# Kernel optimization log

Hardware: AMD Instinct MI355X
Metric: run time of the kernel (lower is better)

## Reference

```python
import jax, jax.numpy as jnp
import numpy as np
from jax import lax

DIM, HEADS, POOL = 512, 8, 16
HD = DIM // HEADS
SCALE = HD ** -0.5


def _cbs(x, w, s, b, d=1, g=1):
    """Conv2d(bias=False, pad=d*(k-1)//2) + folded BN (scale,bias) + SiLU."""
    k = w.shape[-1]
    p = d * (k - 1) // 2
    y = lax.conv_general_dilated(x, w, (1, 1), [(p, p), (p, p)],
                                 rhs_dilation=(d, d), feature_group_count=g,
                                 dimension_numbers=("NCHW", "OIHW", "NCHW"))
    y = y * s[None, :, None, None] + b[None, :, None, None]
    return y * jax.nn.sigmoid(y)  # SiLU


def _forward(x, w01, s01, b01, w02, s02, b02, w03, s03, b03,
             w12, s12, b12, w13, s13, b13, w22, s22, b22, w23, s23, b23,
             w3, s3, b3, wkv, skv, bkv, wfc1, bfc1, wfc2, bfc2):
    bsz, c, h, w = x.shape
    # ---- _MutilScal ----
    a01 = _cbs(x, w01, s01, b01)                       # [b,128,h,w]
    a03 = _cbs(_cbs(a01, w02, s02, b02, d=3, g=128), w03, s03, b03)
    a13 = _cbs(_cbs(a01, w12, s12, b12, d=5, g=128), w13, s13, b13)
    a23 = _cbs(_cbs(a01, w22, s22, b22, d=7, g=128), w23, s23, b23)
    attn = _cbs(a03 + a13 + a23, w3, s3, b3) * x       # [b,512,h,w]
    # AdaptiveAvgPool2d(POOL): exact block mean since h,w divisible by POOL
    pooled = attn.reshape(bsz, c, POOL, h // POOL, POOL, w // POOL).mean(axis=(3, 5))
    kv = _cbs(pooled, wkv, skv, bkv)                   # [b,1024,16,16]
    # ---- pooled cross-attention ----
    n, n1 = h * w, POOL * POOL
    q = x.reshape(bsz, HEADS, HD, n).transpose(0, 1, 3, 2)          # [b,H,n,d]
    kvr = kv.reshape(bsz, 2, HEADS, HD, n1)
    k = kvr[:, 0].transpose(0, 1, 3, 2)                              # [b,H,n1,d]
    v = kvr[:, 1].transpose(0, 1, 3, 2)                              # [b,H,n1,d]
    dots = jnp.einsum("bhnd,bhmd->bhnm", q, k) * SCALE
    a = jax.nn.softmax(dots, axis=-1)
    o = jnp.einsum("bhnm,bhmd->bhnd", a, v)                          # [b,H,n,d]
    attn_out = o.transpose(0, 1, 3, 2).reshape(bsz, c, h, w)
    # ---- SE channel gate ----
    gap = x.mean(axis=(2, 3))                                        # [b,c]
    y = jnp.clip(gap @ wfc1[:, :, 0, 0].T + bfc1, 0.0, 6.0)          # ReLU6
    gate = jax.nn.sigmoid(y @ wfc2[:, :, 0, 0].T + bfc2)             # [b,c]
    c_attn = gate[:, :, None, None] * x
    return attn_out + c_attn


def setup_inputs() -> dict:
    key = jax.random.key(0)
    ks = jax.random.split(key, 32)
    ki = iter(ks)
    f = jnp.float32

    def rn(shape, scale=0.05):
        return (jax.random.normal(next(ki), shape, dtype=f) * scale)

    inp = {"x": jax.random.normal(next(ki), (8, DIM, 64, 64), dtype=f)}
    inp.update(w01=rn((128, 512, 1, 1)), s01=jnp.ones((128,), f), b01=rn((128,)))
    inp.update(w02=rn((128, 1, 3, 3)), s02=jnp.ones((128,), f), b02=rn((128,)))
    inp.update(w03=rn((512, 128, 1, 1)), s03=jnp.ones((512,), f), b03=rn((512,)))
    inp.update(w12=rn((128, 1, 3, 3)), s12=jnp.ones((128,), f), b12=rn((128,)))
    inp.update(w13=rn((512, 128, 1, 1)), s13=jnp.ones((512,), f), b13=rn((512,)))
    inp.update(w22=rn((128, 1, 3, 3)), s22=jnp.ones((128,), f), b22=rn((128,)))
    inp.update(w23=rn((512, 128, 1, 1)), s23=jnp.ones((512,), f), b23=rn((512,)))
    inp.update(w3=rn((512, 512, 1, 1)), s3=jnp.ones((512,), f), b3=rn((512,)))
    inp.update(wkv=rn((1024, 512, 1, 1)), skv=jnp.ones((1024,), f), bkv=rn((1024,)))
    inp.update(wfc1=rn((128, 512, 1, 1)), bfc1=rn((128,)))
    inp.update(wfc2=rn((512, 128, 1, 1)), bfc2=rn((512,)))
    return inp


def reference(x, w01, s01, b01, w02, s02, b02, w03, s03, b03,
              w12, s12, b12, w13, s13, b13, w22, s22, b22, w23, s23, b23,
              w3, s3, b3, wkv, skv, bkv, wfc1, bfc1, wfc2, bfc2):
    return _forward(x, w01, s01, b01, w02, s02, b02, w03, s03, b03,
                    w12, s12, b12, w13, s13, b13, w22, s22, b22, w23, s23, b23,
                    w3, s3, b3, wkv, skv, bkv, wfc1, bfc1, wfc2, bfc2)
```

## Files before the change

kernel.cpp:

```cpp
#include <hip/hip_runtime.h>
#include <cstddef>


static __device__ __forceinline__ float silu_f(float v) {
  return v / (1.f + __expf(-v));
}

typedef __attribute__((ext_vector_type(8))) short short8v;
typedef __attribute__((ext_vector_type(4))) float f32x4;

union FragU { unsigned u[4]; short8v v; uint4 q; };

static __device__ __forceinline__ unsigned short f2bf(float f) {
  unsigned u = __builtin_bit_cast(unsigned, f);
  u += 0x7fffu + ((u >> 16) & 1u);
  return (unsigned short)(u >> 16);
}
static __device__ __forceinline__ unsigned packbf(float lo, float hi) {
  return (unsigned)f2bf(lo) | ((unsigned)f2bf(hi) << 16);
}
static __device__ __forceinline__ float bf_lo(unsigned w) {
  return __builtin_bit_cast(float, w << 16);
}
static __device__ __forceinline__ float bf_hi(unsigned w) {
  return __builtin_bit_cast(float, w & 0xffff0000u);
}

static __device__ __forceinline__ void gload16(const unsigned* gsrc, unsigned* ldst) {
  __builtin_amdgcn_global_load_lds(
      (const __attribute__((address_space(1))) unsigned*)gsrc,
      (__attribute__((address_space(3))) unsigned*)ldst, 16, 0, 0);
}

static __device__ __forceinline__ void stage_tile_g(const unsigned* __restrict__ src,
                                                    unsigned* dst, int tid) {
  gload16(src + 4 * tid, dst + 4 * tid);
  gload16(src + 4 * (tid + 512), dst + 4 * (tid + 512));
}

static __device__ __forceinline__ short8v load_frag4(const unsigned* P, int ksg, int pos) {
  FragU f;
  f.q = *(const uint4*)(P + (((ksg << 7) + pos) << 2));
  return f.v;
}

static __device__ __forceinline__ void xload16(const float* __restrict__ src, int ld,
                                               int tid, float v[16]) {
  const int pos = tid & 127, kg = tid >> 7;
  const float* p = src + pos + (size_t)(kg * 16) * ld;
#pragma unroll
  for (int i = 0; i < 16; ++i) v[i] = p[(size_t)i * ld];
}
static __device__ __forceinline__ void xload16_sum2(const float* __restrict__ a,
                                                    const float* __restrict__ b2, int ld,
                                                    int tid, float v[16]) {
  const int pos = tid & 127, kg = tid >> 7;
  const float* pA = a + pos + (size_t)(kg * 16) * ld;
  const float* pB = b2 + pos + (size_t)(kg * 16) * ld;
#pragma unroll
  for (int i = 0; i < 16; ++i) v[i] = pA[(size_t)i * ld] + pB[(size_t)i * ld];
}
static __device__ __forceinline__ void xwrite16(const float v[16], unsigned* Xp, int tid) {
  const int pos = tid & 127, kg = tid >> 7;
#pragma unroll
  for (int i2 = 0; i2 < 4; ++i2) {
    const int kq = kg * 4 + i2;
    const int r4 = (kq & 3) + ((kq >> 3) << 2);
    const int sub = (kq >> 2) & 1;
    uint2 wv;
    wv.x = packbf(v[i2 * 4 + 0], v[i2 * 4 + 1]);
    wv.y = packbf(v[i2 * 4 + 2], v[i2 * 4 + 3]);
    *(uint2*)(Xp + (((r4 << 7) + pos) << 2) + sub * 2) = wv;
  }
}

static __device__ __forceinline__ void stage_x_pack(const float* __restrict__ src, int ld,
                                                    unsigned* Xp, int tid) {
  float v[16];
  xload16(src, ld, tid, v);
  xwrite16(v, Xp, tid);
}

#define GEMM_IDS                                            \
  const int tid = threadIdx.x;                              \
  const int w = tid >> 6, lane = tid & 63;                  \
  const int g = lane >> 4, nl = lane & 15;                  \
  const int wr = w >> 1, wc = w & 1;

#define GEMM_KSTEP_B(ACC, XB, WB)                                                  \
  _Pragma("unroll")                                                                \
  for (int ks = 0; ks < 2; ++ks) {                                                 \
    const short8v a0 = load_frag4(WB, ks * 4 + g, wr * 32 + nl);                   \
    const short8v a1 = load_frag4(WB, ks * 4 + g, wr * 32 + 16 + nl);              \
    _Pragma("unroll")                                                              \
    for (int jj = 0; jj < 4; ++jj) {                                               \
      const short8v bfr = load_frag4(XB, ks * 4 + g, wc * 64 + jj * 16 + nl);      \
      ACC[0][jj] = __builtin_amdgcn_mfma_f32_16x16x32_bf16(a0, bfr, ACC[0][jj], 0, 0, 0); \
      ACC[1][jj] = __builtin_amdgcn_mfma_f32_16x16x32_bf16(a1, bfr, ACC[1][jj], 0, 0, 0); \
    }                                                                              \
  }

__global__ __launch_bounds__(256)
void prepack_w_kernel(const float* __restrict__ w01, const float* __restrict__ w03,
                      const float* __restrict__ w13, const float* __restrict__ w23,
                      const float* __restrict__ w3, const float* __restrict__ wkv,
                      unsigned* __restrict__ img)
{
  const int t = blockIdx.x;
  const float* W; int K; int tile; unsigned* base;
  if (t < 8)       { W = w01; K = 512; tile = t;      base = img; }
  else if (t < 16) { W = w03; K = 128; tile = t - 8;  base = img + 32768; }
  else if (t < 24) { W = w13; K = 128; tile = t - 16; base = img + 65536; }
  else if (t < 32) { W = w23; K = 128; tile = t - 24; base = img + 98304; }
  else if (t < 64) { W = w3;  K = 512; tile = t - 32; base = img + 131072; }
  else             { W = wkv; K = 512; tile = t - 64; base = img + 262144; }
  const int nk = K >> 6;
  const int to = tile / nk, tk = tile - to * nk;
  unsigned* dst = base + (size_t)tile * 4096;
  for (int wi = threadIdx.x; wi < 4096; wi += 256) {
    const int r4 = wi >> 9, pos = (wi >> 2) & 127, sub = (wi >> 1) & 1, j = wi & 1;
    const int kq = (r4 & 3) + sub * 4 + ((r4 >> 2) << 3);
    const int k = tk * 64 + 4 * kq + 2 * j;
    const int oc = to * 128 + pos;
    dst[wi] = packbf(W[(size_t)oc * K + k], W[(size_t)oc * K + k + 1]);
  }
}

__global__ __launch_bounds__(512)
void gemm_a01_kernel(const float* __restrict__ X, const unsigned* __restrict__ Wimg,
                     const float* __restrict__ sc, const float* __restrict__ bi,
                     unsigned* __restrict__ A01p)
{
  const int b = blockIdx.z, p0 = blockIdx.x * 128;
  GEMM_IDS
  __shared__ unsigned Xp[2][4096], Wp[2][4096];
  const float* Xbase = X + (size_t)b * 512 * 4096 + p0;

  f32x4 acc[2][4];
#pragma unroll
  for (int i = 0; i < 2; ++i)
#pragma unroll
    for (int jj = 0; jj < 4; ++jj) acc[i][jj] = (f32x4){0.f, 0.f, 0.f, 0.f};

  {
    float vx[16];
    xload16(Xbase, 4096, tid, vx);
    stage_tile_g(Wimg, Wp[0], tid);
    xwrite16(vx, Xp[0], tid);
  }
  __syncthreads();

  for (int st = 0; st < 8; ++st) {
    const int cur = st & 1;
    float vn[16];
    if (st < 7) {
      xload16(Xbase + (size_t)((st + 1) * 64) * 4096, 4096, tid, vn);
      stage_tile_g(Wimg + (size_t)(st + 1) * 4096, Wp[cur ^ 1], tid);
    }
    GEMM_KSTEP_B(acc, Xp[cur], Wp[cur])
    if (st < 7) xwrite16(vn, Xp[cur ^ 1], tid);
    __syncthreads();
  }

#pragma unroll
  for (int i = 0; i < 2; ++i) {
    const int base = wr * 32 + i * 16 + 4 * g;
    const float s0_ = sc[base + 0], b0_ = bi[base + 0];
    const float s1_ = sc[base + 1], b1_ = bi[base + 1];
    const float s2_ = sc[base + 2], b2_ = bi[base + 2];
    const float s3_ = sc[base + 3], b3_ = bi[base + 3];
#pragma unroll
    for (int jj = 0; jj < 4; ++jj) {
      const int pos = p0 + wc * 64 + jj * 16 + nl;
      const float v0 = silu_f(s0_ * acc[i][jj][0] + b0_);
      const float v1 = silu_f(s1_ * acc[i][jj][1] + b1_);
      const float v2 = silu_f(s2_ * acc[i][jj][2] + b2_);
      const float v3 = silu_f(s3_ * acc[i][jj][3] + b3_);
      A01p[((size_t)b * 64 + (base >> 1)) * 4096 + pos]     = packbf(v0, v1);
      A01p[((size_t)b * 64 + (base >> 1) + 1) * 4096 + pos] = packbf(v2, v3);
    }
  }
}

__global__ __launch_bounds__(256)
void dwconv_pack_kernel(const unsigned* __restrict__ A01p, unsigned* __restrict__ Timg,
                        const float* __restrict__ w02, const float* __restrict__ s02, const float* __restrict__ b02,
                        const float* __restrict__ w12, const float* __restrict__ s12, const float* __restrict__ b12,
                        const float* __restrict__ w22, const float* __restrict__ s22, const float* __restrict__ b22)
{
  const int br = blockIdx.z;
  const int yb = blockIdx.y;
  const int b = yb >> 4, t16 = yb & 15, kstep = t16 >> 3, mm = t16 & 7;
  const int kq = (mm & 3) + ((mm >> 2) << 3);
  const int cbase = kstep * 64 + kq * 4;
  const int p = blockIdx.x * 256 + threadIdx.x;
  const int y = p >> 6, xx = p & 63;
  const int d = 3 + 2 * br;

  const float* wsel = br == 0 ? w02 : (br == 1 ? w12 : w22);
  const float* ssel = br == 0 ? s02 : (br == 1 ? s12 : s22);
  const float* bsel = br == 0 ? b02 : (br == 1 ? b12 : b22);

  float sum[8] = {};
  const unsigned* plane0 = A01p + ((size_t)b * 64 + (cbase >> 1)) * 4096;

#pragma unroll
  for (int u = -1; u <= 1; ++u) {
    const int yv = y + u * d;
    if ((unsigned)yv < 64u) {
#pragma unroll
      for (int v = -1; v <= 1; ++v) {
        const int xv = xx + v * d;
        if ((unsigned)xv < 64u) {
          const int idx = yv * 64 + xv;
          const int tap = (u + 1) * 3 + (v + 1);
#pragma unroll
          for (int q = 0; q < 4; ++q) {
            const int sub = q >> 1, jw = q & 1;
            const unsigned wv = plane0[(size_t)(sub * 8 + jw) * 4096 + idx];
            const int ch = cbase + sub * 16 + jw * 2;
            sum[q * 2 + 0] += wsel[(ch + 0) * 9 + tap] * bf_lo(wv);
            sum[q * 2 + 1] += wsel[(ch + 1) * 9 + tap] * bf_hi(wv);
          }
        }
      }
    }
  }

  unsigned wout[4];
#pragma unroll
  for (int h = 0; h < 4; ++h) {
    const int ch = cbase + (h >> 1) * 16 + (h & 1) * 2;
    const float va = silu_f(ssel[ch] * sum[h * 2] + bsel[ch]);
    const float vb = silu_f(ssel[ch + 1] * sum[h * 2 + 1] + bsel[ch + 1]);
    wout[h] = packbf(va, vb);
  }
  const int tile = ((br * 8 + b) * 2 + kstep) * 32 + (p >> 7);
  *(uint4*)(Timg + (size_t)tile * 4096 + (((mm << 7) + (p & 127)) << 2)) = *(uint4*)wout;
}

__global__ __launch_bounds__(512)
void gemm3branch_img_kernel(const unsigned* __restrict__ Timg, const unsigned* __restrict__ Wimg3,
                            const float* __restrict__ s0, const float* __restrict__ s1, const float* __restrict__ s2,
                            const float* __restrict__ b0, const float* __restrict__ b1, const float* __restrict__ b2,
                            unsigned* __restrict__ Bimg)
{
  const int b = blockIdx.z, pt = blockIdx.x, oc0 = blockIdx.y * 128;
  GEMM_IDS
  __shared__ unsigned Xp[2][4096], Wp[2][4096];

  float sum[2][4][4] = {};
  f32x4 acc[2][4];
#pragma unroll
  for (int i = 0; i < 2; ++i)
#pragma unroll
    for (int jj = 0; jj < 4; ++jj) acc[i][jj] = (f32x4){0.f, 0.f, 0.f, 0.f};

#define SRC_X3(st) (Timg + (((size_t)(((st) >> 1) * 8 + b) * 2 + ((st) & 1)) * 32 + pt) * 4096)
#define SRC_W3(st) (Wimg3 + (size_t)((st) >> 1) * 32768 + ((size_t)(oc0 >> 7) * 2 + ((st) & 1)) * 4096)

  stage_tile_g(SRC_X3(0), Xp[0], tid);
  stage_tile_g(SRC_W3(0), Wp[0], tid);
  __syncthreads();

  for (int st = 0; st < 6; ++st) {
    const int cur = st & 1;
    if (st < 5) {
      stage_tile_g(SRC_X3(st + 1), Xp[cur ^ 1], tid);
      stage_tile_g(SRC_W3(st + 1), Wp[cur ^ 1], tid);
    }
    GEMM_KSTEP_B(acc, Xp[cur], Wp[cur])
    if (st & 1) {
      const int brn = st >> 1;
      const float* ss = brn == 0 ? s0 : (brn == 1 ? s1 : s2);
      const float* bs = brn == 0 ? b0 : (brn == 1 ? b1 : b2);
#pragma unroll
      for (int i = 0; i < 2; ++i) {
        const int base = oc0 + wr * 32 + i * 16 + 4 * g;
#pragma unroll
        for (int r = 0; r < 4; ++r) {
          const float s = ss[base + r], bb = bs[base + r];
#pragma unroll
          for (int jj = 0; jj < 4; ++jj) {
            sum[i][jj][r] += silu_f(s * acc[i][jj][r] + bb);
            acc[i][jj][r] = 0.f;
          }
        }
      }
    }
    __syncthreads();
  }
#undef SRC_X3
#undef SRC_W3

#pragma unroll
  for (int i = 0; i < 2; ++i) {
    const int ol = wr * 32 + i * 16 + 4 * g;
    const int kstep_g = (oc0 + ol) >> 6;
    const int kin = ol & 63;
    const int kq2 = kin >> 2;
    const int r4 = (kq2 & 3) + ((kq2 >> 3) << 2);
    const int sub = (kq2 >> 2) & 1;
#pragma unroll
    for (int jj = 0; jj < 4; ++jj) {
      const int pos = wc * 64 + jj * 16 + nl;
      uint2 wv;
      wv.x = packbf(sum[i][jj][0], sum[i][jj][1]);
      wv.y = packbf(sum[i][jj][2], sum[i][jj][3]);
      *(uint2*)(Bimg + ((size_t)(b * 8 + kstep_g) * 32 + pt) * 4096 + (((r4 << 7) + pos) << 2) + sub * 2) = wv;
    }
  }
}

__global__ __launch_bounds__(512)
void gemm_pool_img_kernel(const unsigned* __restrict__ Bimg, const unsigned* __restrict__ W3img,
                          const float* __restrict__ sc, const float* __restrict__ bi,
                          const float* __restrict__ xin, float* __restrict__ pooled2)
{
  const int b = blockIdx.z, pt = blockIdx.x, oc0 = blockIdx.y * 128;
  const int p0 = pt * 128;
  const float* xb = xin + (size_t)b * 512 * 4096;
  GEMM_IDS
  __shared__ unsigned Xp[2][4096], Wp[2][4096];

  f32x4 acc[2][4];
#pragma unroll
  for (int i = 0; i < 2; ++i)
#pragma unroll
    for (int jj = 0; jj < 4; ++jj) acc[i][jj] = (f32x4){0.f, 0.f, 0.f, 0.f};

#define SRC_XP(st) (Bimg + ((size_t)(b * 8 + (st)) * 32 + pt) * 4096)
#define SRC_WP(st) (W3img + ((size_t)(oc0 >> 7) * 8 + (st)) * 4096)

  stage_tile_g(SRC_XP(0), Xp[0], tid);
  stage_tile_g(SRC_WP(0), Wp[0], tid);
  __syncthreads();

  for (int st = 0; st < 8; ++st) {
    const int cur = st & 1;
    if (st < 7) {
      stage_tile_g(SRC_XP(st + 1), Xp[cur ^ 1], tid);
      stage_tile_g(SRC_WP(st + 1), Wp[cur ^ 1], tid);
    }
    GEMM_KSTEP_B(acc, Xp[cur], Wp[cur])
    __syncthreads();
  }
#undef SRC_XP
#undef SRC_WP

  float* red = (float*)Wp[0];
  for (int e = tid; e < 2048; e += 512) red[e] = 0.f;
  __syncthreads();

#pragma unroll
  for (int i = 0; i < 2; ++i)
#pragma unroll
    for (int r = 0; r < 4; ++r) {
      const int ol = wr * 32 + i * 16 + 4 * g + r;
      const int oc = oc0 + ol;
      const float s = sc[oc], bb = bi[oc];
#pragma unroll
      for (int jj = 0; jj < 4; ++jj) {
        const int p = p0 + wc * 64 + jj * 16 + nl;
        float val = silu_f(s * acc[i][jj][r] + bb) * xb[(size_t)oc * 4096 + p];
        val += __shfl_xor(val, 1, 64);
        val += __shfl_xor(val, 2, 64);
        if ((nl & 3) == 0) {
          const int col = p & 63;
          atomicAdd(&red[ol * 16 + (col >> 2)], val);
        }
      }
    }
  __syncthreads();

  {
    const int ph = pt >> 1;
    float* pdst = pooled2 + (size_t)(pt & 1) * (8ull * 512 * 256);
    for (int e = tid; e < 2048; e += 512) {
      const int ol = e >> 4, pw = e & 15;
      pdst[((size_t)b * 512 + oc0 + ol) * 256 + ph * 16 + pw] = red[e] * (1.f / 16.f);
    }
  }
}

__global__ __launch_bounds__(512)
void gemm_kv_kernel(const float* __restrict__ pooled2, const unsigned* __restrict__ WKVimg,
                    const float* __restrict__ sc, const float* __restrict__ bi,
                    unsigned* __restrict__ Kimg, unsigned* __restrict__ Vimg)
{
  const int b = blockIdx.z, p0 = blockIdx.x * 128, oc0 = blockIdx.y * 128;
  const float* XbA = pooled2 + (size_t)b * 512 * 256 + p0;
  const float* XbB = XbA + 8ull * 512 * 256;
  GEMM_IDS
  __shared__ unsigned Xp[2][4096], Wp[2][4096];

  f32x4 acc[2][4];
#pragma unroll
  for (int i = 0; i < 2; ++i)
#pragma unroll
    for (int jj = 0; jj < 4; ++jj) acc[i][jj] = (f32x4){0.f, 0.f, 0.f, 0.f};

  {
    float vx[16];
    xload16_sum2(XbA, XbB, 256, tid, vx);
    stage_tile_g(WKVimg + (size_t)(oc0 >> 7) * 8 * 4096, Wp[0], tid);
    xwrite16(vx, Xp[0], tid);
  }
  __syncthreads();

  for (int st = 0; st < 8; ++st) {
    const int cur = st & 1;
    float vn[16];
    if (st < 7) {
      xload16_sum2(XbA + (size_t)((st + 1) * 64) * 256, XbB + (size_t)((st + 1) * 64) * 256,
                   256, tid, vn);
      stage_tile_g(WKVimg + ((size_t)(oc0 >> 7) * 8 + st + 1) * 4096, Wp[cur ^ 1], tid);
    }
    GEMM_KSTEP_B(acc, Xp[cur], Wp[cur])
    if (st < 7) xwrite16(vn, Xp[cur ^ 1], tid);
    __syncthreads();
  }

  const bool isK = (oc0 < 512);
#pragma unroll
  for (int i = 0; i < 2; ++i) {
    const int ocb = oc0 + wr * 32 + i * 16 + 4 * g;
#pragma unroll
    for (int jj = 0; jj < 4; ++jj) {
      const int pos = p0 + wc * 64 + jj * 16 + nl;
      float v[4];
#pragma unroll
      for (int r = 0; r < 4; ++r)
        v[r] = silu_f(sc[ocb + r] * acc[i][jj][r] + bi[ocb + r]);
      const int ch = pos >> 7, ml = pos & 127;
      if (isK) {
        const int h = ocb >> 6, d0 = ocb & 63;
        const int kq = d0 >> 2, sub = (kq >> 2) & 1;
        const int r4 = (kq & 3) + ((kq >> 3) << 2);
        unsigned* t = Kimg + ((size_t)(b * 8 + h) * 2 + ch) * 4096;
        uint2 wv;
        wv.x = packbf(v[0] * 0.125f, v[1] * 0.125f);
        wv.y = packbf(v[2] * 0.125f, v[3] * 0.125f);
        *(uint2*)(t + (((r4 << 7) + ml) << 2) + sub * 2) = wv;
      } else {
        const int h = (ocb - 512) >> 6, d0 = (ocb - 512) & 63;
        unsigned* t = Vimg + ((size_t)(b * 8 + h) * 2 + ch) * 4096;
        float ov[4];
#pragma unroll
        for (int r = 0; r < 4; ++r) ov[r] = __shfl_xor(v[r], 1, 64);
        if ((nl & 1) == 0) {
          const int s = (ml >> 1) & 1, m4 = ml >> 2;
#pragma unroll
          for (int r = 0; r < 4; ++r)
            t[((m4 * 64 + d0 + r) << 1) + s] = packbf(v[r], ov[r]);
        }
      }
    }
  }
}

__global__ __launch_bounds__(256)
void gap_kernel(const float* __restrict__ x, float* __restrict__ gap)
{
  const int bc = blockIdx.x;
  const int tid = threadIdx.x;
  const float* p = x + (size_t)bc * 4096;
  float v = 0.f;
#pragma unroll
  for (int j = 0; j < 16; ++j) v += p[j * 256 + tid];
#pragma unroll
  for (int off = 32; off >= 1; off >>= 1) v += __shfl_down(v, off, 64);
  __shared__ float red[4];
  if ((tid & 63) == 0) red[tid >> 6] = v;
  __syncthreads();
  if (tid == 0) gap[bc] = (red[0] + red[1] + red[2] + red[3]) * (1.f / 4096.f);
}

__global__ __launch_bounds__(512)
void se_kernel(const float* __restrict__ gap,
               const float* __restrict__ wfc1, const float* __restrict__ bfc1,
               const float* __restrict__ wfc2, const float* __restrict__ bfc2,
               float* __restrict__ gate)
{
  const int b = blockIdx.x, tid = threadIdx.x;
  __shared__ float ylds[128];
  if (tid < 128) {
    float a = 0.f;
    for (int c = 0; c < 512; ++c) a += gap[b * 512 + c] * wfc1[tid * 512 + c];
    a += bfc1[tid];
    ylds[tid] = fminf(fmaxf(a, 0.f), 6.f);
  }
  __syncthreads();
  float g = 0.f;
  for (int j = 0; j < 128; ++j) g += ylds[j] * wfc2[tid * 128 + j];
  g += bfc2[tid];
  gate[b * 512 + tid] = 1.f / (1.f + __expf(-g));
}

__global__ __launch_bounds__(512)
void attn_mfma_kernel(const float* __restrict__ x, const unsigned* __restrict__ Kimg,
                      const unsigned* __restrict__ Vimg,
                      const float* __restrict__ gate, float* __restrict__ out)
{
  const int b = blockIdx.z, h = blockIdx.y;
  const int n0 = blockIdx.x * 128;
  const int tid = threadIdx.x;
  const int w = tid >> 6, lane = tid & 63;
  const int g = lane >> 4, nl = lane & 15;

  __shared__ unsigned lds[20480];
  unsigned* Qp = lds;
  unsigned* Kb0 = lds + 4096;
  unsigned* Kb1 = lds + 8192;
  unsigned* Vb0 = lds + 12288;
  unsigned* Vb1 = lds + 16384;
  float* Osm = (float*)(lds + 4096);

  const size_t tbase = (size_t)(b * 8 + h) * 2 * 4096;

  stage_tile_g(Kimg + tbase, Kb0, tid);
  stage_tile_g(Vimg + tbase, Vb0, tid);
  stage_x_pack(x + ((size_t)b * 512 + h * 64) * 4096 + n0, 4096, Qp, tid);
  __syncthreads();
  stage_tile_g(Kimg + tbase + 4096, Kb1, tid);
  stage_tile_g(Vimg + tbase + 4096, Vb1, tid);

  float m_run = -1e30f, l_run = 0.f;
  f32x4 o[4];
#pragma unroll
  for (int i = 0; i < 4; ++i) o[i] = (f32x4){0.f, 0.f, 0.f, 0.f};

#pragma unroll
  for (int ch = 0; ch < 2; ++ch) {
    const unsigned* Kp = ch ? Kb1 : Kb0;
    const unsigned* Vp = ch ? Vb1 : Vb0;

    f32x4 s[8];
#pragma unroll
    for (int mb = 0; mb < 8; ++mb) s[mb] = (f32x4){0.f, 0.f, 0.f, 0.f};
#pragma unroll
    for (int ks = 0; ks < 2; ++ks) {
      const short8v qf = load_frag4(Qp, ks * 4 + g, w * 16 + nl);
#pragma unroll
      for (int mb = 0; mb < 8; ++mb) {
        const short8v kf = load_frag4(Kp, ks * 4 + g, mb * 16 + nl);
        s[mb] = __builtin_amdgcn_mfma_f32_16x16x32_bf16(kf, qf, s[mb], 0, 0, 0);
      }
    }

    float cm = -1e30f;
#pragma unroll
    for (int mb = 0; mb < 8; ++mb)
#pragma unroll
      for (int r = 0; r < 4; ++r) cm = fmaxf(cm, s[mb][r]);
    cm = fmaxf(cm, __shfl_xor(cm, 16, 64));
    cm = fmaxf(cm, __shfl_xor(cm, 32, 64));
    const float mnew = fmaxf(m_run, cm);
    const float corr = __expf(m_run - mnew);
    m_run = mnew;
    float cs = 0.f;
#pragma unroll
    for (int mb = 0; mb < 8; ++mb)
#pragma unroll
      for (int r = 0; r < 4; ++r) {
        const float p = __expf(s[mb][r] - mnew);
        s[mb][r] = p;
        cs += p;
      }
    cs += __shfl_xor(cs, 16, 64);
    cs += __shfl_xor(cs, 32, 64);
    l_run = l_run * corr + cs;
#pragma unroll
    for (int db = 0; db < 4; ++db)
#pragma unroll
      for (int r = 0; r < 4; ++r) o[db][r] *= corr;

#pragma unroll
    for (int ks = 0; ks < 4; ++ks) {
      FragU pf;
      pf.u[0] = packbf(s[2 * ks][0],     s[2 * ks][1]);
      pf.u[1] = packbf(s[2 * ks][2],     s[2 * ks][3]);
      pf.u[2] = packbf(s[2 * ks + 1][0], s[2 * ks + 1][1]);
      pf.u[3] = packbf(s[2 * ks + 1][2], s[2 * ks + 1][3]);
#pragma unroll
      for (int db = 0; db < 4; ++db) {
        FragU vf;
        const uint2 lo = *(const uint2*)(Vp + ((8 * ks + g) * 64 + db * 16 + nl) * 2);
        const uint2 hi = *(const uint2*)(Vp + ((8 * ks + 4 + g) * 64 + db * 16 + nl) * 2);
        vf.u[0] = lo.x; vf.u[1] = lo.y; vf.u[2] = hi.x; vf.u[3] = hi.y;
        o[db] = __builtin_amdgcn_mfma_f32_16x16x32_bf16(vf.v, pf.v, o[db], 0, 0, 0);
      }
    }
    __syncthreads();
  }

  const float inv = 1.f / l_run;
#pragma unroll
  for (int db = 0; db < 4; ++db)
#pragma unroll
    for (int r = 0; r < 4; ++r)
      Osm[(db * 16 + 4 * g + r) * 132 + w * 16 + nl] = o[db][r] * inv;
  __syncthreads();

  {
    const int n = tid & 127, t7 = tid >> 7;
    const int jw = t7 >> 1, half = t7 & 1;
#pragma unroll
    for (int i = 0; i < 16; ++i) {
      const int d = t7 + 4 * i;
      const int r4 = (i & 3) + ((i >> 3) << 2);
      const int sub = (i >> 2) & 1;
      const unsigned xw = Qp[(((r4 << 7) + n) << 2) + sub * 2 + jw];
      const float xv = half ? bf_hi(xw) : bf_lo(xw);
      const int c2 = h * 64 + d;
      const size_t off = ((size_t)b * 512 + c2) * 4096 + n0 + n;
      out[off] = Osm[d * 132 + n] + gate[b * 512 + c2] * xv;
    }
  }
}

extern "C" void kernel_launch(void* const* d_in, const int* in_sizes, int n_in,
                              void* d_out, int out_size, void* d_ws, size_t ws_size,
                              hipStream_t stream)
{
  const float* x    = (const float*)d_in[0];
  const float* w01  = (const float*)d_in[1];
  const float* s01  = (const float*)d_in[2];
  const float* b01  = (const float*)d_in[3];
  const float* w02  = (const float*)d_in[4];
  const float* s02  = (const float*)d_in[5];
  const float* b02  = (const float*)d_in[6];
  const float* w03  = (const float*)d_in[7];
  const float* s03  = (const float*)d_in[8];
  const float* b03  = (const float*)d_in[9];
  const float* w12  = (const float*)d_in[10];
  const float* s12  = (const float*)d_in[11];
  const float* b12  = (const float*)d_in[12];
  const float* w13  = (const float*)d_in[13];
  const float* s13  = (const float*)d_in[14];
  const float* b13  = (const float*)d_in[15];
  const float* w22  = (const float*)d_in[16];
  const float* s22  = (const float*)d_in[17];
  const float* b22  = (const float*)d_in[18];
  const float* w23  = (const float*)d_in[19];
  const float* s23  = (const float*)d_in[20];
  const float* b23  = (const float*)d_in[21];
  const float* w3   = (const float*)d_in[22];
  const float* s3   = (const float*)d_in[23];
  const float* b3   = (const float*)d_in[24];
  const float* wkv  = (const float*)d_in[25];
  const float* skv  = (const float*)d_in[26];
  const float* bkv  = (const float*)d_in[27];
  const float* wfc1 = (const float*)d_in[28];
  const float* bfc1 = (const float*)d_in[29];
  const float* wfc2 = (const float*)d_in[30];
  const float* bfc2 = (const float*)d_in[31];

  float* out = (float*)d_out;
  unsigned* wsu = (unsigned*)d_ws;

  unsigned* Timg    = wsu;
  float*    pooled2 = (float*)(wsu + 6291456);
  unsigned* Kimg    = wsu + 8388608;
  unsigned* Vimg    = wsu + 8912896;
  float*    gapb    = (float*)(wsu + 9437184);
  float*    gateb   = (float*)(wsu + 9441280);
  unsigned* Wimg    = wsu + 9445376;

  unsigned* A01p = (unsigned*)d_out;
  unsigned* Bimg = (unsigned*)d_out;

  prepack_w_kernel<<<128, 256, 0, stream>>>(w01, w03, w13, w23, w3, wkv, Wimg);
  gemm_a01_kernel<<<dim3(32, 1, 8), 512, 0, stream>>>(x, Wimg, s01, b01, A01p);
  dwconv_pack_kernel<<<dim3(16, 128, 3), 256, 0, stream>>>(A01p, Timg,
      w02, s02, b02, w12, s12, b12, w22, s22, b22);
  gemm3branch_img_kernel<<<dim3(32, 4, 8), 512, 0, stream>>>(Timg, Wimg + 32768,
      s03, s13, s23, b03, b13, b23, Bimg);
  gemm_pool_img_kernel<<<dim3(32, 4, 8), 512, 0, stream>>>(Bimg, Wimg + 131072,
      s3, b3, x, pooled2);
  gemm_kv_kernel<<<dim3(2, 8, 8), 512, 0, stream>>>(pooled2, Wimg + 262144, skv, bkv, Kimg, Vimg);
  gap_kernel<<<4096, 256, 0, stream>>>(x, gapb);
  se_kernel<<<8, 512, 0, stream>>>(gapb, wfc1, bfc1, wfc2, bfc2, gateb);
  attn_mfma_kernel<<<dim3(32, 8, 8), 512, 0, stream>>>(x, Kimg, Vimg, gateb, out);
}
```

Before: 235.9 us.

## Keep two tiles in flight with explicit vmcnt waits in GEMM kernels

Measured after the change: 240.4 us. No clear change (+1.9%).

```diff
diff --git a/kernel.cpp b/kernel.cpp
--- a/kernel.cpp
+++ b/kernel.cpp
@@ -10,6 +10,9 @@
 typedef __attribute__((ext_vector_type(4))) float f32x4;
 
 union FragU { unsigned u[4]; short8v v; uint4 q; };
+
+#define VM_WAIT(N) asm volatile("s_waitcnt vmcnt(" #N ")" ::: "memory")
+#define SBAR()     asm volatile("s_barrier" ::: "memory")
 
 static __device__ __forceinline__ unsigned short f2bf(float f) {
   unsigned u = __builtin_bit_cast(unsigned, f);
@@ -261,34 +264,49 @@
 
   stage_tile_g(SRC_X3(0), Xp[0], tid);
   stage_tile_g(SRC_W3(0), Wp[0], tid);
-  __syncthreads();
-
+
+  float4 ssr[3][2], bsr[3][2];
+#pragma unroll
+  for (int brn = 0; brn < 3; ++brn) {
+    const float* ss = brn == 0 ? s0 : (brn == 1 ? s1 : s2);
+    const float* bs = brn == 0 ? b0 : (brn == 1 ? b1 : b2);
+#pragma unroll
+    for (int i = 0; i < 2; ++i) {
+      const int base = oc0 + wr * 32 + i * 16 + 4 * g;
+      ssr[brn][i] = *(const float4*)(ss + base);
+      bsr[brn][i] = *(const float4*)(bs + base);
+    }
+  }
+
+  stage_tile_g(SRC_X3(1), Xp[1], tid);
+  stage_tile_g(SRC_W3(1), Wp[1], tid);
+
+#pragma unroll
   for (int st = 0; st < 6; ++st) {
     const int cur = st & 1;
-    if (st < 5) {
-      stage_tile_g(SRC_X3(st + 1), Xp[cur ^ 1], tid);
-      stage_tile_g(SRC_W3(st + 1), Wp[cur ^ 1], tid);
-    }
+    if (st < 5) { VM_WAIT(4); } else { VM_WAIT(0); }
+    SBAR();
     GEMM_KSTEP_B(acc, Xp[cur], Wp[cur])
     if (st & 1) {
       const int brn = st >> 1;
-      const float* ss = brn == 0 ? s0 : (brn == 1 ? s1 : s2);
-      const float* bs = brn == 0 ? b0 : (brn == 1 ? b1 : b2);
-#pragma unroll
-      for (int i = 0; i < 2; ++i) {
-        const int base = oc0 + wr * 32 + i * 16 + 4 * g;
+#pragma unroll
+      for (int i = 0; i < 2; ++i)
 #pragma unroll
         for (int r = 0; r < 4; ++r) {
-          const float s = ss[base + r], bb = bs[base + r];
+          const float s = ((const float*)&ssr[brn][i])[r];
+          const float bb = ((const float*)&bsr[brn][i])[r];
 #pragma unroll
           for (int jj = 0; jj < 4; ++jj) {
             sum[i][jj][r] += silu_f(s * acc[i][jj][r] + bb);
             acc[i][jj][r] = 0.f;
           }
         }
-      }
-    }
-    __syncthreads();
+    }
+    SBAR();
+    if (st < 4) {
+      stage_tile_g(SRC_X3(st + 2), Xp[cur], tid);
+      stage_tile_g(SRC_W3(st + 2), Wp[cur], tid);
+    }
   }
 #undef SRC_X3
 #undef SRC_W3
@@ -334,16 +352,20 @@
 
   stage_tile_g(SRC_XP(0), Xp[0], tid);
   stage_tile_g(SRC_WP(0), Wp[0], tid);
-  __syncthreads();
-
+  stage_tile_g(SRC_XP(1), Xp[1], tid);
+  stage_tile_g(SRC_WP(1), Wp[1], tid);
+
+#pragma unroll
   for (int st = 0; st < 8; ++st) {
     const int cur = st & 1;
-    if (st < 7) {
-      stage_tile_g(SRC_XP(st + 1), Xp[cur ^ 1], tid);
-      stage_tile_g(SRC_WP(st + 1), Wp[cur ^ 1], tid);
-    }
+    if (st < 7) { VM_WAIT(4); } else { VM_WAIT(0); }
+    SBAR();
     GEMM_KSTEP_B(acc, Xp[cur], Wp[cur])
-    __syncthreads();
+    SBAR();
+    if (st < 6) {
+      stage_tile_g(SRC_XP(st + 2), Xp[cur], tid);
+      stage_tile_g(SRC_WP(st + 2), Wp[cur], tid);
+    }
   }
 #undef SRC_XP
 #undef SRC_WP
```

## Fuse global average pool into pool GEMM epilogue and deepen load pipeline

Applied to the files above, without the earlier changes.

New measurement: 234.3 us. Within noise of the previous version (-0.7%).

```diff
diff --git a/kernel.cpp b/kernel.cpp
--- a/kernel.cpp
+++ b/kernel.cpp
@@ -10,6 +10,9 @@
 typedef __attribute__((ext_vector_type(4))) float f32x4;
 
 union FragU { unsigned u[4]; short8v v; uint4 q; };
+
+#define VM_WAIT(N) asm volatile("s_waitcnt vmcnt(" #N ")" ::: "memory")
+#define SBAR()     asm volatile("s_barrier" ::: "memory")
 
 static __device__ __forceinline__ unsigned short f2bf(float f) {
   unsigned u = __builtin_bit_cast(unsigned, f);
@@ -315,7 +318,8 @@
 __global__ __launch_bounds__(512)
 void gemm_pool_img_kernel(const unsigned* __restrict__ Bimg, const unsigned* __restrict__ W3img,
                           const float* __restrict__ sc, const float* __restrict__ bi,
-                          const float* __restrict__ xin, float* __restrict__ pooled2)
+                          const float* __restrict__ xin, float* __restrict__ pooled2,
+                          float* __restrict__ gapb)
 {
   const int b = blockIdx.z, pt = blockIdx.x, oc0 = blockIdx.y * 128;
   const int p0 = pt * 128;
@@ -334,24 +338,30 @@
 
   stage_tile_g(SRC_XP(0), Xp[0], tid);
   stage_tile_g(SRC_WP(0), Wp[0], tid);
-  __syncthreads();
-
+  stage_tile_g(SRC_XP(1), Xp[1], tid);
+  stage_tile_g(SRC_WP(1), Wp[1], tid);
+
+#pragma unroll
   for (int st = 0; st < 8; ++st) {
     const int cur = st & 1;
-    if (st < 7) {
-      stage_tile_g(SRC_XP(st + 1), Xp[cur ^ 1], tid);
-      stage_tile_g(SRC_WP(st + 1), Wp[cur ^ 1], tid);
-    }
+    if (st < 7) { VM_WAIT(4); } else { VM_WAIT(0); }
+    SBAR();
     GEMM_KSTEP_B(acc, Xp[cur], Wp[cur])
-    __syncthreads();
+    SBAR();
+    if (st < 6) {
+      stage_tile_g(SRC_XP(st + 2), Xp[cur], tid);
+      stage_tile_g(SRC_WP(st + 2), Wp[cur], tid);
+    }
   }
 #undef SRC_XP
 #undef SRC_WP
 
-  float* red = (float*)Wp[0];
-  for (int e = tid; e < 2048; e += 512) red[e] = 0.f;
-  __syncthreads();
-
+  float* red  = (float*)Wp[0];
+  float* gred = red + 2048;
+  for (int e = tid; e < 2176; e += 512) red[e] = 0.f;
+  __syncthreads();
+
+  float xsum[2][4] = {};
 #pragma unroll
   for (int i = 0; i < 2; ++i)
 #pragma unroll
@@ -362,7 +372,9 @@
 #pragma unroll
       for (int jj = 0; jj < 4; ++jj) {
         const int p = p0 + wc * 64 + jj * 16 + nl;
-        float val = silu_f(s * acc[i][jj][r] + bb) * xb[(size_t)oc * 4096 + p];
+        const float xv = xb[(size_t)oc * 4096 + p];
+        xsum[i][r] += xv;
+        float val = silu_f(s * acc[i][jj][r] + bb) * xv;
         val += __shfl_xor(val, 1, 64);
         val += __shfl_xor(val, 2, 64);
         if ((nl & 3) == 0) {
@@ -371,6 +383,18 @@
         }
       }
     }
+#pragma unroll
+  for (int i = 0; i < 2; ++i)
+#pragma unroll
+    for (int r = 0; r < 4; ++r) {
+      float v = xsum[i][r];
+      v += __shfl_xor(v, 1, 64);
+      v += __shfl_xor(v, 2, 64);
+      v += __shfl_xor(v, 4, 64);
+      v += __shfl_xor(v, 8, 64);
+      if (nl == 0)
+        atomicAdd(&gred[wr * 32 + i * 16 + 4 * g + r], v);
+    }
   __syncthreads();
 
   {
@@ -380,6 +404,8 @@
       const int ol = e >> 4, pw = e & 15;
       pdst[((size_t)b * 512 + oc0 + ol) * 256 + ph * 16 + pw] = red[e] * (1.f / 16.f);
     }
+    if (tid < 128)
+      atomicAdd(&gapb[b * 512 + oc0 + tid], gred[tid]);
   }
 }
 
@@ -459,23 +485,6 @@
   }
 }
 
-__global__ __launch_bounds__(256)
-void gap_kernel(const float* __restrict__ x, float* __restrict__ gap)
-{
-  const int bc = blockIdx.x;
-  const int tid = threadIdx.x;
-  const float* p = x + (size_t)bc * 4096;
-  float v = 0.f;
-#pragma unroll
-  for (int j = 0; j < 16; ++j) v += p[j * 256 + tid];
-#pragma unroll
-  for (int off = 32; off >= 1; off >>= 1) v += __shfl_down(v, off, 64);
-  __shared__ float red[4];
-  if ((tid & 63) == 0) red[tid >> 6] = v;
-  __syncthreads();
-  if (tid == 0) gap[bc] = (red[0] + red[1] + red[2] + red[3]) * (1.f / 4096.f);
-}
-
 __global__ __launch_bounds__(512)
 void se_kernel(const float* __restrict__ gap,
                const float* __restrict__ wfc1, const float* __restrict__ bfc1,
@@ -487,7 +496,7 @@
   if (tid < 128) {
     float a = 0.f;
     for (int c = 0; c < 512; ++c) a += gap[b * 512 + c] * wfc1[tid * 512 + c];
-    a += bfc1[tid];
+    a = a * (1.f / 4096.f) + bfc1[tid];
     ylds[tid] = fminf(fmaxf(a, 0.f), 6.f);
   }
   __syncthreads();
@@ -676,10 +685,10 @@
       w02, s02, b02, w12, s12, b12, w22, s22, b22);
   gemm3branch_img_kernel<<<dim3(32, 4, 8), 512, 0, stream>>>(Timg, Wimg + 32768,
       s03, s13, s23, b03, b13, b23, Bimg);
+  hipMemsetAsync(gapb, 0, 4096 * sizeof(float), stream);
   gemm_pool_img_kernel<<<dim3(32, 4, 8), 512, 0, stream>>>(Bimg, Wimg + 131072,
-      s3, b3, x, pooled2);
+      s3, b3, x, pooled2, gapb);
   gemm_kv_kernel<<<dim3(2, 8, 8), 512, 0, stream>>>(pooled2, Wimg + 262144, skv, bkv, Kimg, Vimg);
-  gap_kernel<<<4096, 256, 0, stream>>>(x, gapb);
   se_kernel<<<8, 512, 0, stream>>>(gapb, wfc1, bfc1, wfc2, bfc2, gateb);
   attn_mfma_kernel<<<dim3(32, 8, 8), 512, 0, stream>>>(x, Kimg, Vimg, gateb, out);
 }
```
